# Kernel tuning notes

Hardware: AMD Instinct MI355X
Metric: run time of the kernel (lower is better)

The kernel has to match this reference:

```python
import jax, jax.numpy as jnp
import numpy as np

N = 98304        # total nodes (= 16384 graphs * act_dim 6)
E = 1572864      # edges (avg degree 16)
C = 64           # in_channels
H = 32           # hidden_size
ACT = 6          # act_dim


def setup_inputs() -> dict:
    key = jax.random.key(0)
    ks = jax.random.split(key, 11)
    s = lambda fan: 1.0 / np.sqrt(fan)
    return {
        "state": jax.random.normal(ks[0], (N, C), jnp.float32),
        "edge_index": jax.random.randint(ks[1], (2, E), 0, N, dtype=jnp.int64),
        "conv_W": jax.random.normal(ks[2], (C, C), jnp.float32) * s(C),
        "conv_b": jax.random.normal(ks[3], (C,), jnp.float32) * 0.01,
        "W1": jax.random.normal(ks[4], (C, H), jnp.float32) * s(C),
        "b1": jax.random.normal(ks[5], (H,), jnp.float32) * 0.01,
        "W2": jax.random.normal(ks[6], (H, H), jnp.float32) * s(H),
        "b2": jax.random.normal(ks[7], (H,), jnp.float32) * 0.01,
        "W3": jax.random.normal(ks[8], (H, 1), jnp.float32) * s(H),
        "b3": jax.random.normal(ks[9], (1,), jnp.float32) * 0.01,
    }


def gcn_conv(x, edge_index, W, b):
    # PyG GCNConv: add self-loops, symmetric normalization D^-1/2 (A+I) D^-1/2 (X W) + b
    loops = jnp.arange(N, dtype=edge_index.dtype)
    src = jnp.concatenate([edge_index[0], loops])  # [E+N]
    dst = jnp.concatenate([edge_index[1], loops])  # [E+N]
    deg = jax.ops.segment_sum(jnp.ones(E + N, x.dtype), dst, num_segments=N)
    dinv = jax.lax.rsqrt(deg)                      # deg >= 1 due to self-loops
    norm = dinv[src] * dinv[dst]                   # [E+N]
    h = x @ W                                      # [N, C]
    msg = h[src] * norm[:, None]                   # gather + scale
    return jax.ops.segment_sum(msg, dst, num_segments=N) + b


def reference(state, edge_index, conv_W, conv_b, W1, b1, W2, b2, W3, b3):
    out = jax.nn.relu(gcn_conv(state, edge_index, conv_W, conv_b))
    x = out + state                                # residual
    x = x.reshape(-1, ACT, C)                      # [num_graphs, act_dim, C]
    x = jax.nn.relu(x @ W1 + b1)
    x = jax.nn.relu(x @ W2 + b2)
    x = jax.nn.softplus(x @ W3 + b3)
    concentration = x.squeeze(-1) + 1e-20          # [num_graphs, act_dim]
    return concentration
```

## Files before the change

kernel.cpp:

```cpp
#include <hip/hip_runtime.h>
#include <math.h>

#define Nn 98304
#define Ee 1572864
#define Cc 64
#define Hh 32
#define TT 128
#define NT (Nn / TT)
#define HB 256
#define EPB (Ee / HB)
#define CAPT 2560
#define GN 64


__device__ __forceinline__ int detect64(const void* ei) {
    const unsigned int* u = (const unsigned int*)ei;
    int is64 = 1;
    #pragma unroll
    for (int i = 0; i < 16; ++i) is64 &= (u[2 * i + 1] == 0u);
    return is64;
}

__device__ __forceinline__ int load_idx(const void* ei, long e, int is64) {
    if (is64) return (int)((const long long*)ei)[e];
    return ((const int*)ei)[e];
}

__device__ __forceinline__ unsigned short f2bf(float x) {
    union { float f; unsigned int u; } v; v.f = x;
    unsigned int r = v.u + 0x7FFFu + ((v.u >> 16) & 1u);
    return (unsigned short)(r >> 16);
}
__device__ __forceinline__ float bf2f(unsigned short h) {
    union { unsigned int u; float f; } v; v.u = ((unsigned int)h) << 16;
    return v.f;
}

__global__ __launch_bounds__(1024) void k_bucket(const void* __restrict__ ei,
                                                 unsigned int* __restrict__ aux,
                                                 unsigned int* __restrict__ ebuf) {
    __shared__ unsigned int hl[NT];
    __shared__ unsigned int off[NT];
    int t = threadIdx.x, b = blockIdx.x;
    if (t < NT) hl[t] = 0;
    __syncthreads();
    int is64 = detect64(ei);
    long e0 = (long)b * EPB;
    #pragma unroll
    for (int i = 0; i < EPB / 1024; ++i) {
        int d = load_idx(ei, (long)Ee + e0 + i * 1024 + t, is64);
        atomicAdd(&hl[d >> 7], 1u);
    }
    __syncthreads();
    if (t < NT) off[t] = hl[t];
    __syncthreads();
    for (int s = 1; s < NT; s <<= 1) {
        unsigned int v = (t < NT && t >= s) ? off[t - s] : 0u;
        __syncthreads();
        if (t < NT) off[t] += v;
        __syncthreads();
    }
    if (t < NT) {
        unsigned int ex = off[t] - hl[t];
        aux[(long)b * NT + t] = ex | (hl[t] << 16);
        off[t] = ex;
    }
    __syncthreads();
    #pragma unroll
    for (int i = 0; i < EPB / 1024; ++i) {
        long e = e0 + i * 1024 + t;
        int s = load_idx(ei, e, is64);
        int d = load_idx(ei, (long)Ee + e, is64);
        unsigned int pos = atomicAdd(&off[d >> 7], 1u);
        ebuf[(long)b * EPB + pos] = (unsigned int)s | ((unsigned int)(d & (TT - 1)) << 17);
    }
}

__global__ __launch_bounds__(256) void k_nodecnt(const unsigned int* __restrict__ aux,
                                                 const unsigned int* __restrict__ ebuf,
                                                 unsigned int* __restrict__ rowOff,
                                                 unsigned int* __restrict__ rowEnd,
                                                 float* __restrict__ dinv,
                                                 unsigned int* __restrict__ srcs) {
    __shared__ unsigned int stage[CAPT];
    __shared__ unsigned int rb[HB];
    __shared__ unsigned int cnt[TT];
    __shared__ unsigned int sc[TT];
    __shared__ unsigned int cur[TT];
    int t = threadIdx.x, tile = blockIdx.x;
    unsigned int av = aux[(long)t * NT + tile];
    unsigned int roff = av & 0xFFFFu, rcnt = av >> 16;
    rb[t] = rcnt;
    __syncthreads();
    for (int s = 1; s < HB; s <<= 1) {
        unsigned int v = (t >= s) ? rb[t - s] : 0u;
        __syncthreads();
        rb[t] += v;
        __syncthreads();
    }
    unsigned int mybase = rb[t] - rcnt;
    for (unsigned int i = 0; i < rcnt; ++i)
        stage[mybase + i] = ebuf[(long)t * EPB + roff + i];
    if (t < TT) cnt[t] = 0;
    __syncthreads();
    int total = (int)rb[HB - 1];
    for (int i = t; i < total; i += 256)
        atomicAdd(&cnt[stage[i] >> 17], 1u);
    __syncthreads();
    if (t < TT) sc[t] = cnt[t];
    __syncthreads();
    #pragma unroll
    for (int off = 1; off < TT; off <<= 1) {
        unsigned int v = (t >= off && t < TT) ? sc[t - off] : 0u;
        __syncthreads();
        if (t < TT) sc[t] += v;
        __syncthreads();
    }
    if (t < TT) {
        unsigned int start = (unsigned int)(tile * CAPT) + sc[t] - cnt[t];
        rowOff[(long)tile * TT + t] = start;
        rowEnd[(long)tile * TT + t] = start + cnt[t];
        cur[t] = start;
        dinv[(long)tile * TT + t] = rsqrtf((float)(cnt[t] + 1));
    }
    __syncthreads();
    for (int i = t; i < total; i += 256) {
        unsigned int u = stage[i];
        unsigned int pos = atomicAdd(&cur[u >> 17], 1u);
        srcs[pos] = u & 0x1FFFFu;
    }
}

__global__ __launch_bounds__(256) void k_gemm(const float* __restrict__ state,
                                              const float* __restrict__ W,
                                              const float* __restrict__ dinv,
                                              unsigned short* __restrict__ gb) {
    __shared__ float Wl[64 * 64];
    __shared__ float Al[64 * 68];
    int t = threadIdx.x;
    long n0 = (long)blockIdx.x * 64;

    const float4* W4 = (const float4*)W;
    float4* Wl4 = (float4*)Wl;
    #pragma unroll
    for (int i = 0; i < 4; ++i) Wl4[i * 256 + t] = W4[i * 256 + t];

    const float4* S4 = (const float4*)(state) + n0 * 16;
    #pragma unroll
    for (int i = 0; i < 4; ++i) {
        int f4 = t + i * 256;
        int r = f4 >> 4, k0 = (f4 & 15) * 4;
        *(float4*)(Al + r * 68 + k0) = S4[f4];
    }
    __syncthreads();

    int r0 = (t >> 4) * 4;
    int c0 = (t & 15) * 4;
    float acc[4][4] = {{0.f}};
    #pragma unroll
    for (int kk = 0; kk < 64; kk += 4) {
        float4 a4[4], w4[4];
        #pragma unroll
        for (int i = 0; i < 4; ++i) a4[i] = *(const float4*)(Al + (r0 + i) * 68 + kk);
        #pragma unroll
        for (int j = 0; j < 4; ++j) w4[j] = *(const float4*)(Wl + (kk + j) * 64 + c0);
        const float* aa = (const float*)a4;
        const float* ww = (const float*)w4;
        #pragma unroll
        for (int i = 0; i < 4; ++i)
            #pragma unroll
            for (int j = 0; j < 4; ++j) {
                float av = aa[i * 4 + j];
                #pragma unroll
                for (int c = 0; c < 4; ++c)
                    acc[i][c] = fmaf(av, ww[j * 4 + c], acc[i][c]);
            }
    }
    #pragma unroll
    for (int i = 0; i < 4; ++i) {
        long n = n0 + r0 + i;
        float dv = dinv[n];
        ushort4 o;
        o.x = f2bf(acc[i][0] * dv); o.y = f2bf(acc[i][1] * dv);
        o.z = f2bf(acc[i][2] * dv); o.w = f2bf(acc[i][3] * dv);
        *(ushort4*)(gb + n * 64 + c0) = o;
    }
}

__global__ __launch_bounds__(512) void k_gf(const unsigned int* __restrict__ rowOff,
                                            const unsigned int* __restrict__ rowEnd,
                                            const unsigned int* __restrict__ srcs,
                                            const unsigned short* __restrict__ gb,
                                            const float* __restrict__ dinv,
                                            const float* __restrict__ state,
                                            const float* __restrict__ conv_b,
                                            const float* __restrict__ W1,
                                            const float* __restrict__ b1,
                                            const float* __restrict__ W2,
                                            const float* __restrict__ b2,
                                            const float* __restrict__ W3,
                                            const float* __restrict__ b3,
                                            float* __restrict__ out) {
    __shared__ float sa[GN * 68];
    __shared__ float hs[GN * 34];
    __shared__ float sW1[Cc * Hh];
    __shared__ float sW2[Hh * Hh];
    __shared__ float sW3[Hh], sb1[Hh], sb2[Hh], scb[Cc];
    __shared__ float sb3;
    int t = threadIdx.x;
    int wave = t >> 6, lane = t & 63;
    long n0 = (long)blockIdx.x * GN;

    for (int i = t; i < Cc * Hh; i += 512) sW1[i] = W1[i];
    for (int i = t; i < Hh * Hh; i += 512) sW2[i] = W2[i];
    if (t < Hh) { sW3[t] = W3[t]; sb1[t] = b1[t]; sb2[t] = b2[t]; }
    if (t >= 64 && t < 128) scb[t - 64] = conv_b[t - 64];
    if (t == 511) sb3 = b3[0];

    #pragma unroll
    for (int jj = 0; jj < 8; ++jj) {
        int j = wave * 8 + jj;
        long n = n0 + j;
        int start = (int)rowOff[n];
        int end = (int)rowEnd[n];
        float acc = bf2f(gb[n * 64 + lane]);
        for (int base = start; base < end; base += 64) {
            int m = min(64, end - base);
            int sv = (lane < m) ? (int)srcs[base + lane] : 0;
            int q = 0;
            for (; q + 8 <= m; q += 8) {
                int s0 = __shfl(sv, q,     64);
                int s1 = __shfl(sv, q + 1, 64);
                int s2 = __shfl(sv, q + 2, 64);
                int s3 = __shfl(sv, q + 3, 64);
                int s4 = __shfl(sv, q + 4, 64);
                int s5 = __shfl(sv, q + 5, 64);
                int s6 = __shfl(sv, q + 6, 64);
                int s7 = __shfl(sv, q + 7, 64);
                float v0 = bf2f(gb[(long)s0 * 64 + lane]);
                float v1 = bf2f(gb[(long)s1 * 64 + lane]);
                float v2 = bf2f(gb[(long)s2 * 64 + lane]);
                float v3 = bf2f(gb[(long)s3 * 64 + lane]);
                float v4 = bf2f(gb[(long)s4 * 64 + lane]);
                float v5 = bf2f(gb[(long)s5 * 64 + lane]);
                float v6 = bf2f(gb[(long)s6 * 64 + lane]);
                float v7 = bf2f(gb[(long)s7 * 64 + lane]);
                acc += ((v0 + v1) + (v2 + v3)) + ((v4 + v5) + (v6 + v7));
            }
            for (; q < m; ++q) {
                int s = __shfl(sv, q, 64);
                acc += bf2f(gb[(long)s * 64 + lane]);
            }
        }
        sa[j * 68 + lane] = acc * dinv[n];
    }
    __syncthreads();

    {
        int j = t >> 3, o = t & 7;
        long n = n0 + j;
        int k0 = o * 8;
        const float4* sp4 = (const float4*)(state + n * 64 + k0);
        float4 s0 = sp4[0], s1 = sp4[1];
        float* r = sa + j * 68 + k0;
        r[0] = fmaxf(r[0] + scb[k0 + 0], 0.f) + s0.x;
        r[1] = fmaxf(r[1] + scb[k0 + 1], 0.f) + s0.y;
        r[2] = fmaxf(r[2] + scb[k0 + 2], 0.f) + s0.z;
        r[3] = fmaxf(r[3] + scb[k0 + 3], 0.f) + s0.w;
        r[4] = fmaxf(r[4] + scb[k0 + 4], 0.f) + s1.x;
        r[5] = fmaxf(r[5] + scb[k0 + 5], 0.f) + s1.y;
        r[6] = fmaxf(r[6] + scb[k0 + 6], 0.f) + s1.z;
        r[7] = fmaxf(r[7] + scb[k0 + 7], 0.f) + s1.w;
    }
    __syncthreads();

    {
        int j = t >> 3, o = t & 7;
        int c0 = o * 4;
        float a0 = sb1[c0], a1 = sb1[c0 + 1], a2 = sb1[c0 + 2], a3 = sb1[c0 + 3];
        #pragma unroll
        for (int k = 0; k < Cc; ++k) {
            float xv = sa[j * 68 + k];
            float4 w = *(const float4*)(sW1 + k * Hh + c0);
            a0 = fmaf(xv, w.x, a0); a1 = fmaf(xv, w.y, a1);
            a2 = fmaf(xv, w.z, a2); a3 = fmaf(xv, w.w, a3);
        }
        float* r = hs + j * 34 + c0;
        r[0] = fmaxf(a0, 0.f); r[1] = fmaxf(a1, 0.f);
        r[2] = fmaxf(a2, 0.f); r[3] = fmaxf(a3, 0.f);
    }
    __syncthreads();

    {
        int j = t >> 3, o = t & 7;
        int c0 = o * 4;
        float a0 = sb2[c0], a1 = sb2[c0 + 1], a2 = sb2[c0 + 2], a3 = sb2[c0 + 3];
        #pragma unroll
        for (int k = 0; k < Hh; ++k) {
            float xv = hs[j * 34 + k];
            float4 w = *(const float4*)(sW2 + k * Hh + c0);
            a0 = fmaf(xv, w.x, a0); a1 = fmaf(xv, w.y, a1);
            a2 = fmaf(xv, w.z, a2); a3 = fmaf(xv, w.w, a3);
        }
        float* r = sa + j * 68 + c0;
        r[0] = fmaxf(a0, 0.f); r[1] = fmaxf(a1, 0.f);
        r[2] = fmaxf(a2, 0.f); r[3] = fmaxf(a3, 0.f);
    }
    __syncthreads();

    if (t < GN) {
        float y = sb3;
        #pragma unroll
        for (int k = 0; k < Hh; ++k) y = fmaf(sa[t * 68 + k], sW3[k], y);
        float sp = fmaxf(y, 0.f) + log1pf(expf(-fabsf(y)));
        out[n0 + t] = sp + 1e-20f;
    }
}

extern "C" void kernel_launch(void* const* d_in, const int* in_sizes, int n_in,
                              void* d_out, int out_size, void* d_ws, size_t ws_size,
                              hipStream_t stream) {
    const float* state  = (const float*)d_in[0];
    const void*  ei     = d_in[1];
    const float* conv_W = (const float*)d_in[2];
    const float* conv_b = (const float*)d_in[3];
    const float* W1 = (const float*)d_in[4];
    const float* b1 = (const float*)d_in[5];
    const float* W2 = (const float*)d_in[6];
    const float* b2 = (const float*)d_in[7];
    const float* W3 = (const float*)d_in[8];
    const float* b3 = (const float*)d_in[9];
    float* out = (float*)d_out;

    float*          dinv   = (float*)d_ws;
    unsigned short* gb     = (unsigned short*)(dinv + Nn);
    unsigned int*   rowOff = (unsigned int*)(gb + (size_t)Nn * 64);
    unsigned int*   rowEnd = rowOff + Nn;
    unsigned int*   aux    = rowEnd + Nn;
    unsigned int*   ebuf   = aux + (size_t)HB * NT;
    unsigned int*   srcs   = ebuf + Ee;

    k_bucket<<<HB, 1024, 0, stream>>>(ei, aux, ebuf);
    k_nodecnt<<<NT, 256, 0, stream>>>(aux, ebuf, rowOff, rowEnd, dinv, srcs);
    k_gemm<<<Nn / 64, 256, 0, stream>>>(state, conv_W, dinv, gb);
    k_gf<<<Nn / GN, 512, 0, stream>>>(rowOff, rowEnd, srcs, gb, dinv, state, conv_b,
                                      W1, b1, W2, b2, W3, b3, out);
}
```

Measured before the change: 195.8 us.

## Gather neighbor rows with 8-lane groups and 16-byte bf16 loads per node

The aggregation loop in the fused MLP kernel now assigns each wave's eight nodes to eight 8-lane subgroups that run concurrently. Each lane loads a uint4 holding 8 bf16 channels, replacing the one-bf16-per-lane loads where the whole wave walked the nodes in turn. This cuts the number of load instructions, keeps more gathers in flight, and drops the shuffles. In exchange, lanes in a wave diverge when node degrees differ, and each lane reads the source indices itself.

```diff
diff --git a/kernel.cpp b/kernel.cpp
--- a/kernel.cpp
+++ b/kernel.cpp
@@ -34,6 +34,29 @@
 __device__ __forceinline__ float bf2f(unsigned short h) {
     union { unsigned int u; float f; } v; v.u = ((unsigned int)h) << 16;
     return v.f;
+}
+
+__device__ __forceinline__ void acc_u4(float a[8], uint4 u) {
+    union { unsigned int i; float f; } w;
+    w.i = u.x << 16;         a[0] += w.f;
+    w.i = u.x & 0xFFFF0000u; a[1] += w.f;
+    w.i = u.y << 16;         a[2] += w.f;
+    w.i = u.y & 0xFFFF0000u; a[3] += w.f;
+    w.i = u.z << 16;         a[4] += w.f;
+    w.i = u.z & 0xFFFF0000u; a[5] += w.f;
+    w.i = u.w << 16;         a[6] += w.f;
+    w.i = u.w & 0xFFFF0000u; a[7] += w.f;
+}
+__device__ __forceinline__ void set_u4(float a[8], uint4 u) {
+    union { unsigned int i; float f; } w;
+    w.i = u.x << 16;         a[0] = w.f;
+    w.i = u.x & 0xFFFF0000u; a[1] = w.f;
+    w.i = u.y << 16;         a[2] = w.f;
+    w.i = u.y & 0xFFFF0000u; a[3] = w.f;
+    w.i = u.z << 16;         a[4] = w.f;
+    w.i = u.z & 0xFFFF0000u; a[5] = w.f;
+    w.i = u.w << 16;         a[6] = w.f;
+    w.i = u.w & 0xFFFF0000u; a[7] = w.f;
 }
 
 __global__ __launch_bounds__(1024) void k_bucket(const void* __restrict__ ei,
@@ -217,42 +240,45 @@
     if (t >= 64 && t < 128) scb[t - 64] = conv_b[t - 64];
     if (t == 511) sb3 = b3[0];
 
-    #pragma unroll
-    for (int jj = 0; jj < 8; ++jj) {
-        int j = wave * 8 + jj;
+    {
+        int g = lane >> 3;
+        int cs = lane & 7;
+        int j = wave * 8 + g;
         long n = n0 + j;
-        int start = (int)rowOff[n];
+        int ptr = (int)rowOff[n];
         int end = (int)rowEnd[n];
-        float acc = bf2f(gb[n * 64 + lane]);
-        for (int base = start; base < end; base += 64) {
-            int m = min(64, end - base);
-            int sv = (lane < m) ? (int)srcs[base + lane] : 0;
-            int q = 0;
-            for (; q + 8 <= m; q += 8) {
-                int s0 = __shfl(sv, q,     64);
-                int s1 = __shfl(sv, q + 1, 64);
-                int s2 = __shfl(sv, q + 2, 64);
-                int s3 = __shfl(sv, q + 3, 64);
-                int s4 = __shfl(sv, q + 4, 64);
-                int s5 = __shfl(sv, q + 5, 64);
-                int s6 = __shfl(sv, q + 6, 64);
-                int s7 = __shfl(sv, q + 7, 64);
-                float v0 = bf2f(gb[(long)s0 * 64 + lane]);
-                float v1 = bf2f(gb[(long)s1 * 64 + lane]);
-                float v2 = bf2f(gb[(long)s2 * 64 + lane]);
-                float v3 = bf2f(gb[(long)s3 * 64 + lane]);
-                float v4 = bf2f(gb[(long)s4 * 64 + lane]);
-                float v5 = bf2f(gb[(long)s5 * 64 + lane]);
-                float v6 = bf2f(gb[(long)s6 * 64 + lane]);
-                float v7 = bf2f(gb[(long)s7 * 64 + lane]);
-                acc += ((v0 + v1) + (v2 + v3)) + ((v4 + v5) + (v6 + v7));
-            }
-            for (; q < m; ++q) {
-                int s = __shfl(sv, q, 64);
-                acc += bf2f(gb[(long)s * 64 + lane]);
-            }
+        float dv = dinv[n];
+        const uint4* gb4 = (const uint4*)gb;
+
+        float a[8];
+        set_u4(a, gb4[n * 8 + cs]);
+
+        int cnt = end - ptr;
+        while (cnt >= 4) {
+            int s0 = (int)srcs[ptr];
+            int s1 = (int)srcs[ptr + 1];
+            int s2 = (int)srcs[ptr + 2];
+            int s3 = (int)srcs[ptr + 3];
+            uint4 u0 = gb4[(long)s0 * 8 + cs];
+            uint4 u1 = gb4[(long)s1 * 8 + cs];
+            uint4 u2 = gb4[(long)s2 * 8 + cs];
+            uint4 u3 = gb4[(long)s3 * 8 + cs];
+            acc_u4(a, u0); acc_u4(a, u1); acc_u4(a, u2); acc_u4(a, u3);
+            ptr += 4; cnt -= 4;
         }
-        sa[j * 68 + lane] = acc * dinv[n];
+        while (cnt > 0) {
+            int s0 = (int)srcs[ptr];
+            uint4 u0 = gb4[(long)s0 * 8 + cs];
+            acc_u4(a, u0);
+            ++ptr; --cnt;
+        }
+
+        float* r = sa + j * 68 + cs * 8;
+        float4 lo, hi;
+        lo.x = a[0] * dv; lo.y = a[1] * dv; lo.z = a[2] * dv; lo.w = a[3] * dv;
+        hi.x = a[4] * dv; hi.y = a[5] * dv; hi.z = a[6] * dv; hi.w = a[7] * dv;
+        *(float4*)r = lo;
+        *(float4*)(r + 4) = hi;
     }
     __syncthreads();
 
```

Measured after the change: 169.1 us. -13.6%, faster.
